# Performance work log

Measured on AMD Instinct MI355X. Metric: run time of the kernel, lower is better.

Reference implementation:

```python
import jax, jax.numpy as jnp
import numpy as np

# Static graph-batch geometry: B graphs, N nodes each (contiguous), DEG avg degree.
B, N, DEG = 128, 512, 16
GID, GH = 128, 128      # g_in_dim, g_hidden_dim
CID, CE = 64, 64        # c_in_dim, c_embed_dim
HAZ = 256               # haz_dim
K1, K2, K3 = 256, 128, 64


def _gcn(x, src, dst, mask, W, b, n):
    # GCN layer with self loops over masked (surviving) nodes; masked-out nodes contribute nothing.
    h = x @ W  # [n, GH]
    w = mask[src] * mask[dst]                                  # edge alive iff both endpoints alive
    deg = mask + jax.ops.segment_sum(w, dst, num_segments=n)    # +mask = self loop
    dinv = jax.lax.rsqrt(jnp.maximum(deg, 1.0))
    norm = w * dinv[src] * dinv[dst]
    agg = jax.ops.segment_sum(norm[:, None] * h[src], dst, num_segments=n)
    self_term = h * (mask * dinv * dinv)[:, None]               # self-loop norm = 1/deg
    return (agg + self_term + b) * mask[:, None]


def _pool(x, mask, p, k):
    # Score-based top-k pooling (MVPool score -> gate -> keep top ratio per graph), mask-based for static shapes.
    score = jax.nn.sigmoid((x @ p) / jnp.sqrt(jnp.sum(p * p)))  # [B*N]
    s = jnp.where(mask > 0, score, -jnp.inf).reshape(B, N)
    _, idx = jax.lax.top_k(s, k)                                 # [B, k]
    new_mask = jnp.zeros((B, N), x.dtype).at[jnp.arange(B)[:, None], idx].set(1.0).reshape(-1)
    x = x * (score * new_mask)[:, None]
    return x, new_mask


def _readout(x, mask):
    # readout='both': concat(global_max_pool, global_mean_pool) per graph.
    xm = x.reshape(B, N, -1)
    m = mask.reshape(B, N, 1)
    mx = jnp.max(jnp.where(m > 0, xm, -1e30), axis=1)
    avg = jnp.sum(xm * m, axis=1) / jnp.maximum(jnp.sum(m, axis=1), 1.0)
    return jnp.concatenate([mx, avg], axis=1)


def _forward(x, inp_c, src, dst, W1, b1, W2, b2, W3, b3, p1, p2, p3, We, Wa, ba, Wb, bb, Wc):
    n = B * N
    mask = jnp.ones((n,), x.dtype)
    x = jax.nn.relu(_gcn(x, src, dst, mask, W1, b1, n))
    x, mask = _pool(x, mask, p1, K1)
    x1 = _readout(x, mask)
    x = jax.nn.relu(_gcn(x, src, dst, mask, W2, b2, n))
    x, mask = _pool(x, mask, p2, K2)
    x2 = _readout(x, mask)
    x = jax.nn.relu(_gcn(x, src, dst, mask, W3, b3, n))
    x, mask = _pool(x, mask, p3, K3)
    x3 = _readout(x, mask)
    hg = jax.nn.relu(x1) + jax.nn.relu(x2) + jax.nn.relu(x3)     # [B, 2*GH]
    embed = jax.nn.relu(inp_c @ We)                               # [B, CE]
    fusion = jnp.concatenate([embed, hg], axis=1)                 # [B, 320]
    h = jax.nn.relu(fusion @ Wa + ba)                             # dropout skipped (eval mode)
    h = jax.nn.relu(h @ Wb + bb)
    return h @ Wc                                                 # out_dim=1 -> Identity


def setup_inputs() -> dict:
    key = jax.random.key(0)
    ks = jax.random.split(key, 16)
    n = B * N
    x = jax.random.normal(ks[0], (n, GID), jnp.float32)
    inp_c = jax.random.normal(ks[1], (B, CID), jnp.float32)
    offs = (jnp.arange(B, dtype=jnp.int32) * N)[:, None]
    src = (jax.random.randint(ks[2], (B, N * DEG), 0, N, jnp.int32) + offs).reshape(-1)
    dst = (jax.random.randint(ks[3], (B, N * DEG), 0, N, jnp.int32) + offs).reshape(-1)
    edge_index = jnp.stack([src, dst])
    batch = jnp.arange(n, dtype=jnp.int32) // N
    def lin(k, i, o):
        return jax.random.normal(k, (i, o), jnp.float32) / np.float32(np.sqrt(i))
    return dict(
        x=x, inp_c=inp_c, edge_index=edge_index, batch=batch,
        W1=lin(ks[4], GID, GH), b1=jnp.zeros((GH,), jnp.float32),
        W2=lin(ks[5], GH, GH), b2=jnp.zeros((GH,), jnp.float32),
        W3=lin(ks[6], GH, GH), b3=jnp.zeros((GH,), jnp.float32),
        p1=jax.random.normal(ks[7], (GH,), jnp.float32),
        p2=jax.random.normal(ks[8], (GH,), jnp.float32),
        p3=jax.random.normal(ks[9], (GH,), jnp.float32),
        We=lin(ks[10], CID, CE),
        Wa=lin(ks[11], 2 * GH + CE, HAZ), ba=jnp.zeros((HAZ,), jnp.float32),
        Wb=lin(ks[12], HAZ, HAZ // 2), bb=jnp.zeros((HAZ // 2,), jnp.float32),
        Wc=lin(ks[13], HAZ // 2, 1),
    )


def reference(x, inp_c, edge_index, batch, W1, b1, W2, b2, W3, b3, p1, p2, p3, We, Wa, ba, Wb, bb, Wc):
    # batch is implicitly arange(n)//N (contiguous equal-size graphs); reductions use the reshape form.
    src, dst = edge_index[0], edge_index[1]
    return _forward(x, inp_c, src, dst, W1, b1, W2, b2, W3, b3, p1, p2, p3, We, Wa, ba, Wb, bb, Wc)
```

## Files before the change

kernel.cpp:

```cpp
#include <hip/hip_runtime.h>
#include <math.h>

#define NNODE 65536
#define NEDGE 1048576
#define NGRAPH 128
#define NPG 512
#define EPG 8192

typedef _Float16 f16x8 __attribute__((ext_vector_type(8)));
typedef _Float16 f16x4 __attribute__((ext_vector_type(4)));
typedef float f32x4 __attribute__((ext_vector_type(4)));


__global__ __launch_bounds__(512) void k_csr(const int* __restrict__ srcE, const int* __restrict__ dstE,
                                             int* __restrict__ rp, int* __restrict__ csr,
                                             float* __restrict__ gate, int* __restrict__ alive,
                                             float* __restrict__ dinv) {
    __shared__ int cnt[512];
    __shared__ int tmp[512];
    int g = blockIdx.x, t = threadIdx.x;
    int nd = g * NPG + t;
    cnt[t] = 0;
    gate[nd] = 1.f;
    alive[nd] = nd;
    __syncthreads();
    int ebase = g * EPG;
    int dl[16];
    for (int i = 0; i < 16; ++i) {
        int e = ebase + t + i * 512;
        int d = dstE[e] - g * NPG;
        dl[i] = d;
        atomicAdd(&cnt[d], 1);
    }
    __syncthreads();
    int v = cnt[t], incl = v;
    dinv[nd] = rsqrtf(1.f + (float)v);
    for (int off = 1; off < 512; off <<= 1) {
        tmp[t] = incl; __syncthreads();
        if (t >= off) incl += tmp[t - off];
        __syncthreads();
    }
    int excl = incl - v;
    rp[nd] = ebase + excl;
    if (g == NGRAPH - 1 && t == 511) rp[NNODE] = NEDGE;
    __syncthreads();
    cnt[t] = excl;
    __syncthreads();
    for (int i = 0; i < 16; ++i) {
        int e = ebase + t + i * 512;
        int pos = atomicAdd(&cnt[dl[i]], 1);
        csr[ebase + pos] = srcE[e];
    }
}


__global__ __launch_bounds__(256) void k_wconv(const float* __restrict__ W0, const float* __restrict__ W1,
                                               const float* __restrict__ W2, _Float16* __restrict__ wh,
                                               _Float16* __restrict__ wl) {
    int l = blockIdx.x >> 6;
    int e = (blockIdx.x & 63) * 256 + threadIdx.x;
    const float* W = (l == 0) ? W0 : (l == 1) ? W1 : W2;
    int k = e >> 7, n = e & 127;
    float w = W[e];
    _Float16 hi = (_Float16)w;
    _Float16 lo = (_Float16)((w - (float)hi) * 2048.0f);
    int nt = n >> 4, nn = n & 15, ks = k >> 5, quad = (k & 31) >> 3, j = k & 7;
    int off = l * 16384 + ((nt * 4 + ks) * 64 + (quad * 16 + nn)) * 8 + j;
    wh[off] = hi;
    wl[off] = lo;
}


#define CVT8(hi8, lo8, a0, a1, a2, a3, a4, a5, a6, a7)                         \
    {                                                                           \
        _Float16 q0 = (_Float16)a0, q1 = (_Float16)a1, q2 = (_Float16)a2,       \
                 q3 = (_Float16)a3, q4 = (_Float16)a4, q5 = (_Float16)a5,       \
                 q6 = (_Float16)a6, q7 = (_Float16)a7;                          \
        hi8 = (f16x8){q0, q1, q2, q3, q4, q5, q6, q7};                          \
        lo8 = (f16x8){(_Float16)((a0 - (float)q0) * 2048.f),                    \
                      (_Float16)((a1 - (float)q1) * 2048.f),                    \
                      (_Float16)((a2 - (float)q2) * 2048.f),                    \
                      (_Float16)((a3 - (float)q3) * 2048.f),                    \
                      (_Float16)((a4 - (float)q4) * 2048.f),                    \
                      (_Float16)((a5 - (float)q5) * 2048.f),                    \
                      (_Float16)((a6 - (float)q6) * 2048.f),                    \
                      (_Float16)((a7 - (float)q7) * 2048.f)};                   \
    }

__global__ __launch_bounds__(256, 2) void k_gemm(const float* __restrict__ x0, const _Float16* __restrict__ xh,
                                                 const _Float16* __restrict__ xl, const _Float16* __restrict__ wh,
                                                 const _Float16* __restrict__ wl, const float* __restrict__ gate,
                                                 const int* __restrict__ alive, float* __restrict__ h,
                                                 int srcF32) {
    __shared__ _Float16 aH[128 * 72];
    __shared__ _Float16 aL[128 * 72];
    __shared__ _Float16 bH[8192];
    __shared__ _Float16 bL[8192];
    int t = threadIdx.x;
    int lane = t & 63;
    int wv = t >> 6;
    int quad = lane >> 4, mm = lane & 15;
    int rowbase = blockIdx.x * 128;

    f32x4 accH[2][8], accM[2][8];
    for (int a = 0; a < 2; ++a)
        for (int b = 0; b < 8; ++b) {
            accH[a][b] = (f32x4){0.f, 0.f, 0.f, 0.f};
            accM[a][b] = (f32x4){0.f, 0.f, 0.f, 0.f};
        }

    for (int kh = 0; kh < 2; ++kh) {
        if (kh) __syncthreads();
        for (int pp = 0; pp < 4; ++pp) {
            int seg = t + pp * 256;
            int nt = seg >> 7, ksl = (seg >> 6) & 1, ln = seg & 63;
            int goff = ((nt * 4 + kh * 2 + ksl) * 64 + ln) * 8;
            *(uint4*)(bH + seg * 8) = *(const uint4*)(wh + goff);
            *(uint4*)(bL + seg * 8) = *(const uint4*)(wl + goff);
        }
        for (int pp = 0; pp < 4; ++pp) {
            int c = t + pp * 256;
            int r = c >> 3, ch = c & 7;
            int node = alive[rowbase + r];
            size_t src = (size_t)node * 128 + kh * 64 + ch * 8;
            f16x8 hi8, lo8;
            if (srcF32) {
                float4 v0 = *(const float4*)(x0 + src);
                float4 v1 = *(const float4*)(x0 + src + 4);
                CVT8(hi8, lo8, v0.x, v0.y, v0.z, v0.w, v1.x, v1.y, v1.z, v1.w);
            } else {
                hi8 = *(const f16x8*)(xh + src);
                lo8 = *(const f16x8*)(xl + src);
            }
            *(f16x8*)(aH + r * 72 + ch * 8) = hi8;
            *(f16x8*)(aL + r * 72 + ch * 8) = lo8;
        }
        __syncthreads();

        for (int ksl = 0; ksl < 2; ++ksl) {
            f16x8 Ah[2], Al[2];
            for (int mt = 0; mt < 2; ++mt) {
                int row = wv * 32 + mt * 16 + mm;
                Ah[mt] = *(const f16x8*)(aH + row * 72 + ksl * 32 + quad * 8);
                Al[mt] = *(const f16x8*)(aL + row * 72 + ksl * 32 + quad * 8);
            }
            for (int nt = 0; nt < 8; ++nt) {
                f16x8 Bh = *(const f16x8*)(bH + ((nt * 2 + ksl) * 64 + lane) * 8);
                f16x8 Bl = *(const f16x8*)(bL + ((nt * 2 + ksl) * 64 + lane) * 8);
                for (int mt = 0; mt < 2; ++mt) {
                    accH[mt][nt] = __builtin_amdgcn_mfma_f32_16x16x32_f16(Ah[mt], Bh, accH[mt][nt], 0, 0, 0);
                    accM[mt][nt] = __builtin_amdgcn_mfma_f32_16x16x32_f16(Ah[mt], Bl, accM[mt][nt], 0, 0, 0);
                    accM[mt][nt] = __builtin_amdgcn_mfma_f32_16x16x32_f16(Al[mt], Bh, accM[mt][nt], 0, 0, 0);
                }
            }
        }
    }

    for (int mt = 0; mt < 2; ++mt)
        for (int i = 0; i < 4; ++i) {
            int rl = wv * 32 + mt * 16 + quad * 4 + i;
            int node = alive[rowbase + rl];
            float g = gate[node];
            float* hr = h + (size_t)node * 128 + mm;
            for (int nt = 0; nt < 8; ++nt)
                hr[nt * 16] = g * (accH[mt][nt][i] + accM[mt][nt][i] * (1.f / 2048.f));
        }
}


__global__ __launch_bounds__(256) void k_agg(const float* __restrict__ h, const float* __restrict__ dinv,
                                             const int* __restrict__ rp, const int* __restrict__ csr,
                                             const int* __restrict__ alive, const float* __restrict__ bias,
                                             const float* __restrict__ p, _Float16* __restrict__ xh,
                                             _Float16* __restrict__ xl, float* __restrict__ score, int Kp) {
    __shared__ float2 nb[8][16];
    int t = threadIdx.x;
    int slot = t >> 5;
    int lane32 = t & 31;
    int half = slot & 1;
    int g = blockIdx.x & 127;
    int chunk = blockIdx.x >> 7;
    int idx = chunk * 8 + slot;

    int d = alive[g * Kp + idx];
    int jb = rp[d];
    int je = rp[d + 1];
    int deg = je - jb;

    int sid = 0; float wv = 0.f; bool livej = false;
    if (lane32 < 16 && lane32 < deg) {
        sid = csr[jb + lane32];
        wv = dinv[sid];
        livej = (wv != 0.f);
    }
    unsigned long long bal = __ballot(livej);
    unsigned hm = (unsigned)((bal >> (half * 32)) & 0xFFFFu);
    int cnt = __popc(hm);
    if (livej) {
        int pos = __popc(hm & ((1u << lane32) - 1));
        nb[slot][pos] = make_float2(wv, __int_as_float(sid));
    }

    float dvd = dinv[d];
    float4 hd = *(const float4*)(h + (size_t)d * 128 + lane32 * 4);
    float4 a0, a1;
    a0.x = dvd * hd.x; a0.y = dvd * hd.y; a0.z = dvd * hd.z; a0.w = dvd * hd.w;
    a1.x = 0.f; a1.y = 0.f; a1.z = 0.f; a1.w = 0.f;

    int j = 0;
    for (; j + 2 <= cnt; j += 2) {
        float2 n0 = nb[slot][j];
        float2 n1 = nb[slot][j + 1];
        int s0 = __float_as_int(n0.y);
        int s1 = __float_as_int(n1.y);
        float4 h0 = *(const float4*)(h + (size_t)s0 * 128 + lane32 * 4);
        float4 h1 = *(const float4*)(h + (size_t)s1 * 128 + lane32 * 4);
        a0.x = fmaf(n0.x, h0.x, a0.x); a0.y = fmaf(n0.x, h0.y, a0.y);
        a0.z = fmaf(n0.x, h0.z, a0.z); a0.w = fmaf(n0.x, h0.w, a0.w);
        a1.x = fmaf(n1.x, h1.x, a1.x); a1.y = fmaf(n1.x, h1.y, a1.y);
        a1.z = fmaf(n1.x, h1.z, a1.z); a1.w = fmaf(n1.x, h1.w, a1.w);
    }
    if (j < cnt) {
        float2 n0 = nb[slot][j];
        int s0 = __float_as_int(n0.y);
        float4 h0 = *(const float4*)(h + (size_t)s0 * 128 + lane32 * 4);
        a0.x = fmaf(n0.x, h0.x, a0.x); a0.y = fmaf(n0.x, h0.y, a0.y);
        a0.z = fmaf(n0.x, h0.z, a0.z); a0.w = fmaf(n0.x, h0.w, a0.w);
    }
    for (int j2 = jb + 16; j2 < je; ++j2) {
        int s2 = csr[j2];
        float w2 = dinv[s2];
        float4 h2 = *(const float4*)(h + (size_t)s2 * 128 + lane32 * 4);
        a0.x = fmaf(w2, h2.x, a0.x); a0.y = fmaf(w2, h2.y, a0.y);
        a0.z = fmaf(w2, h2.z, a0.z); a0.w = fmaf(w2, h2.w, a0.w);
    }

    float4 b4 = *(const float4*)(bias + lane32 * 4);
    float4 o;
    o.x = fmaxf(fmaf(dvd, a0.x + a1.x, b4.x), 0.f);
    o.y = fmaxf(fmaf(dvd, a0.y + a1.y, b4.y), 0.f);
    o.z = fmaxf(fmaf(dvd, a0.z + a1.z, b4.z), 0.f);
    o.w = fmaxf(fmaf(dvd, a0.w + a1.w, b4.w), 0.f);

    _Float16 q0 = (_Float16)o.x, q1 = (_Float16)o.y, q2 = (_Float16)o.z, q3 = (_Float16)o.w;
    f16x4 oh = {q0, q1, q2, q3};
    f16x4 ol = {(_Float16)((o.x - (float)q0) * 2048.f), (_Float16)((o.y - (float)q1) * 2048.f),
                (_Float16)((o.z - (float)q2) * 2048.f), (_Float16)((o.w - (float)q3) * 2048.f)};
    *(f16x4*)(xh + (size_t)d * 128 + lane32 * 4) = oh;
    *(f16x4*)(xl + (size_t)d * 128 + lane32 * 4) = ol;

    float4 p4 = *(const float4*)(p + lane32 * 4);
    float ps = o.x * p4.x + o.y * p4.y + o.z * p4.z + o.w * p4.w;
    float q = p4.x * p4.x + p4.y * p4.y + p4.z * p4.z + p4.w * p4.w;
    for (int m = 16; m >= 1; m >>= 1) {
        ps += __shfl_xor(ps, m);
        q += __shfl_xor(q, m);
    }
    if (lane32 == 0) score[d] = 1.f / (1.f + expf(-ps * rsqrtf(q)));
}


__global__ __launch_bounds__(512) void k_pool(const _Float16* __restrict__ xh, const _Float16* __restrict__ xl,
                                              const float* __restrict__ score, float* __restrict__ gate,
                                              int* __restrict__ alive, float* __restrict__ hg,
                                              const int* __restrict__ rp, const int* __restrict__ csr,
                                              float* __restrict__ dinv, int K, int last) {
    __shared__ float s[512];
    __shared__ int ad[256];
    __shared__ float ag[256];
    __shared__ float red[1024];
    __shared__ int m_new[512];
    __shared__ int scnt;
    int t = threadIdx.x, g = blockIdx.x;
    int gbase = g * NPG;
    int d = gbase + t;

    float odv = dinv[d];
    int m = odv > 0.f;
    float sc = score[d];
    if (t == 0) scnt = 0;
    s[t] = m ? sc : -__builtin_inff();
    __syncthreads();
    for (int k2 = 2; k2 <= 512; k2 <<= 1)
        for (int j = k2 >> 1; j > 0; j >>= 1) {
            int ixj = t ^ j;
            if (ixj > t) {
                float a = s[t], bv = s[ixj];
                bool sw = ((t & k2) == 0) ? (a < bv) : (a > bv);
                if (sw) { s[t] = bv; s[ixj] = a; }
            }
            __syncthreads();
        }
    float thr = s[K - 1];
    int nm = (m && sc >= thr) ? 1 : 0;
    gate[d] = nm ? sc : 0.f;
    m_new[t] = nm;
    if (nm) {
        int pos = atomicAdd(&scnt, 1);
        if (pos < K) {
            alive[g * K + pos] = d;
            ad[pos] = d;
            ag[pos] = sc;
        }
    }
    __syncthreads();

    if (!last) {
        float nd = 0.f;
        if (nm) {
            int jb = rp[d], je = rp[d + 1];
            int sum = 0;
            for (int j = jb; j < je; ++j) sum += m_new[csr[j] - gbase];
            nd = rsqrtf(1.f + (float)sum);
        }
        dinv[d] = nd;
    }

    int f = t & 127, c = t >> 7;
    float mx = 0.f, sm = 0.f;
#define REC(node) ((float)xh[(size_t)(node)*128 + f] + (float)xl[(size_t)(node)*128 + f] * (1.f / 2048.f))
    for (int j = c; j < K; j += 16) {
        float v0 = REC(ad[j]) * ag[j];
        float v1 = REC(ad[j + 4]) * ag[j + 4];
        float v2 = REC(ad[j + 8]) * ag[j + 8];
        float v3 = REC(ad[j + 12]) * ag[j + 12];
        mx = fmaxf(fmaxf(fmaxf(mx, v0), fmaxf(v1, v2)), v3);
        sm += v0 + v1 + v2 + v3;
    }
#undef REC
    red[t] = mx; red[512 + t] = sm;
    __syncthreads();
    if (c == 0) {
        for (int cc = 1; cc < 4; ++cc) {
            mx = fmaxf(mx, red[cc * 128 + f]);
            sm += red[512 + cc * 128 + f];
        }
        hg[g * 256 + f] += mx;
        hg[g * 256 + 128 + f] += sm / (float)K;
    }
}


__global__ __launch_bounds__(256) void k_mlp(const float* __restrict__ inp_c, const float* __restrict__ hg,
                                             const float* __restrict__ We, const float* __restrict__ Wa,
                                             const float* __restrict__ ba, const float* __restrict__ Wb,
                                             const float* __restrict__ bb, const float* __restrict__ Wc,
                                             float* __restrict__ out) {
    __shared__ float fus[320];
    __shared__ float h1[256];
    __shared__ float h2[128];
    int t = threadIdx.x, g = blockIdx.x;
    if (t < 64) {
        float a = 0.f;
        for (int j = 0; j < 64; ++j) a = fmaf(inp_c[g * 64 + j], We[j * 64 + t], a);
        fus[t] = fmaxf(a, 0.f);
    }
    fus[64 + t] = hg[g * 256 + t];
    __syncthreads();
    {
        float a = ba[t];
        for (int j = 0; j < 320; ++j) a = fmaf(fus[j], Wa[j * 256 + t], a);
        h1[t] = fmaxf(a, 0.f);
    }
    __syncthreads();
    if (t < 128) {
        float a = bb[t];
        for (int j = 0; j < 256; ++j) a = fmaf(h1[j], Wb[j * 128 + t], a);
        h2[t] = fmaxf(a, 0.f);
    }
    __syncthreads();
    if (t == 0) {
        float a = 0.f;
        for (int j = 0; j < 128; ++j) a = fmaf(h2[j], Wc[j], a);
        out[g] = a;
    }
}


extern "C" void kernel_launch(void* const* d_in, const int* in_sizes, int n_in,
                              void* d_out, int out_size, void* d_ws, size_t ws_size,
                              hipStream_t stream) {
    (void)in_sizes; (void)n_in; (void)out_size; (void)ws_size;
    const float* x_in  = (const float*)d_in[0];
    const float* inp_c = (const float*)d_in[1];
    const int*   ei    = (const int*)d_in[2];
    const int* srcE = ei;
    const int* dstE = ei + NEDGE;
    const float* Wl[3] = {(const float*)d_in[4], (const float*)d_in[6], (const float*)d_in[8]};
    const float* bl[3] = {(const float*)d_in[5], (const float*)d_in[7], (const float*)d_in[9]};
    const float* Pl[3] = {(const float*)d_in[10], (const float*)d_in[11], (const float*)d_in[12]};
    const float* We = (const float*)d_in[13];
    const float* Wa = (const float*)d_in[14];
    const float* ba = (const float*)d_in[15];
    const float* Wb = (const float*)d_in[16];
    const float* bb = (const float*)d_in[17];
    const float* Wc = (const float*)d_in[18];
    float* out = (float*)d_out;

    char* w = (char*)d_ws;
    size_t off = 0;
    auto alloc = [&](size_t bytes) -> void* {
        void* p = w + off;
        off = (off + bytes + 255) & ~(size_t)255;
        return p;
    };
    int*   rp    = (int*)alloc((NNODE + 1) * 4);
    int*   csr   = (int*)alloc(NEDGE * 4);
    float* dinv  = (float*)alloc(NNODE * 4);
    float* gate  = (float*)alloc(NNODE * 4);
    float* score = (float*)alloc(NNODE * 4);
    int*   alive = (int*)alloc(NNODE * 4);
    float* hbuf  = (float*)alloc((size_t)NNODE * 128 * 4);
    _Float16* xh = (_Float16*)alloc((size_t)NNODE * 128 * 2);
    _Float16* xl = (_Float16*)alloc((size_t)NNODE * 128 * 2);
    float* hg    = (float*)alloc(NGRAPH * 256 * 4);
    _Float16* wfh = (_Float16*)alloc(3 * 16384 * 2);
    _Float16* wfl = (_Float16*)alloc(3 * 16384 * 2);

    hipMemsetAsync(hg, 0, NGRAPH * 256 * 4, stream);
    k_wconv<<<192, 256, 0, stream>>>(Wl[0], Wl[1], Wl[2], wfh, wfl);
    k_csr<<<NGRAPH, 512, 0, stream>>>(srcE, dstE, rp, csr, gate, alive, dinv);

    const int rows_in[3] = {65536, 32768, 16384};
    const int Ks[3] = {256, 128, 64};
    const int Kp[3] = {512, 256, 128};
    for (int l = 0; l < 3; ++l) {
        k_gemm<<<rows_in[l] / 128, 256, 0, stream>>>(x_in, xh, xl, wfh + l * 16384, wfl + l * 16384,
                                                     gate, alive, hbuf, l == 0);
        k_agg<<<rows_in[l] / 8, 256, 0, stream>>>(hbuf, dinv, rp, csr, alive, bl[l], Pl[l],
                                                  xh, xl, score, Kp[l]);
        k_pool<<<NGRAPH, 512, 0, stream>>>(xh, xl, score, gate, alive, hg,
                                           rp, csr, dinv, Ks[l], l == 2);
    }
    k_mlp<<<NGRAPH, 256, 0, stream>>>(inp_c, hg, We, Wa, ba, Wb, bb, Wc, out);
}
```

Baseline: 309.8 us.

## Replace bitonic sort top-k with radix histogram select; widen aggregation neighbor staging

The pooling kernel no longer runs a full 512-element bitonic sort, which needs about 45 block barriers, to find the K-th largest score. It now builds a 1024-bucket histogram on the top bits of each score, prefix-scans it to locate the bucket holding the K-th value, and ranks only the candidates in that bucket. The aggregation kernel stages up to 32 neighbors per node in shared memory instead of 16, and unrolls the gather loop by 4 with four accumulators to keep more loads in flight. The risks are shared-memory atomic contention when many scores fall in one bucket, and a quadratic candidate ranking if scores cluster. Tied scores at the threshold could also be handled differently from the sort.

```diff
diff --git a/kernel.cpp b/kernel.cpp
--- a/kernel.cpp
+++ b/kernel.cpp
@@ -173,7 +173,7 @@
                                              const int* __restrict__ alive, const float* __restrict__ bias,
                                              const float* __restrict__ p, _Float16* __restrict__ xh,
                                              _Float16* __restrict__ xl, float* __restrict__ score, int Kp) {
-    __shared__ float2 nb[8][16];
+    __shared__ float2 nb[8][32];
     int t = threadIdx.x;
     int slot = t >> 5;
     int lane32 = t & 31;
@@ -188,13 +188,13 @@
     int deg = je - jb;
 
     int sid = 0; float wv = 0.f; bool livej = false;
-    if (lane32 < 16 && lane32 < deg) {
+    if (lane32 < deg) {
         sid = csr[jb + lane32];
         wv = dinv[sid];
         livej = (wv != 0.f);
     }
     unsigned long long bal = __ballot(livej);
-    unsigned hm = (unsigned)((bal >> (half * 32)) & 0xFFFFu);
+    unsigned hm = (unsigned)(bal >> (half * 32));
     int cnt = __popc(hm);
     if (livej) {
         int pos = __popc(hm & ((1u << lane32) - 1));
@@ -203,31 +203,37 @@
 
     float dvd = dinv[d];
     float4 hd = *(const float4*)(h + (size_t)d * 128 + lane32 * 4);
-    float4 a0, a1;
+    float4 a0, a1, a2, a3;
     a0.x = dvd * hd.x; a0.y = dvd * hd.y; a0.z = dvd * hd.z; a0.w = dvd * hd.w;
-    a1.x = 0.f; a1.y = 0.f; a1.z = 0.f; a1.w = 0.f;
+    a1 = make_float4(0.f, 0.f, 0.f, 0.f);
+    a2 = a1; a3 = a1;
 
     int j = 0;
-    for (; j + 2 <= cnt; j += 2) {
+    for (; j + 4 <= cnt; j += 4) {
         float2 n0 = nb[slot][j];
         float2 n1 = nb[slot][j + 1];
-        int s0 = __float_as_int(n0.y);
-        int s1 = __float_as_int(n1.y);
-        float4 h0 = *(const float4*)(h + (size_t)s0 * 128 + lane32 * 4);
-        float4 h1 = *(const float4*)(h + (size_t)s1 * 128 + lane32 * 4);
+        float2 n2 = nb[slot][j + 2];
+        float2 n3 = nb[slot][j + 3];
+        float4 h0 = *(const float4*)(h + (size_t)__float_as_int(n0.y) * 128 + lane32 * 4);
+        float4 h1 = *(const float4*)(h + (size_t)__float_as_int(n1.y) * 128 + lane32 * 4);
+        float4 h2 = *(const float4*)(h + (size_t)__float_as_int(n2.y) * 128 + lane32 * 4);
+        float4 h3 = *(const float4*)(h + (size_t)__float_as_int(n3.y) * 128 + lane32 * 4);
         a0.x = fmaf(n0.x, h0.x, a0.x); a0.y = fmaf(n0.x, h0.y, a0.y);
         a0.z = fmaf(n0.x, h0.z, a0.z); a0.w = fmaf(n0.x, h0.w, a0.w);
         a1.x = fmaf(n1.x, h1.x, a1.x); a1.y = fmaf(n1.x, h1.y, a1.y);
         a1.z = fmaf(n1.x, h1.z, a1.z); a1.w = fmaf(n1.x, h1.w, a1.w);
-    }
-    if (j < cnt) {
+        a2.x = fmaf(n2.x, h2.x, a2.x); a2.y = fmaf(n2.x, h2.y, a2.y);
+        a2.z = fmaf(n2.x, h2.z, a2.z); a2.w = fmaf(n2.x, h2.w, a2.w);
+        a3.x = fmaf(n3.x, h3.x, a3.x); a3.y = fmaf(n3.x, h3.y, a3.y);
+        a3.z = fmaf(n3.x, h3.z, a3.z); a3.w = fmaf(n3.x, h3.w, a3.w);
+    }
+    for (; j < cnt; ++j) {
         float2 n0 = nb[slot][j];
-        int s0 = __float_as_int(n0.y);
-        float4 h0 = *(const float4*)(h + (size_t)s0 * 128 + lane32 * 4);
+        float4 h0 = *(const float4*)(h + (size_t)__float_as_int(n0.y) * 128 + lane32 * 4);
         a0.x = fmaf(n0.x, h0.x, a0.x); a0.y = fmaf(n0.x, h0.y, a0.y);
         a0.z = fmaf(n0.x, h0.z, a0.z); a0.w = fmaf(n0.x, h0.w, a0.w);
     }
-    for (int j2 = jb + 16; j2 < je; ++j2) {
+    for (int j2 = jb + 32; j2 < je; ++j2) {
         int s2 = csr[j2];
         float w2 = dinv[s2];
         float4 h2 = *(const float4*)(h + (size_t)s2 * 128 + lane32 * 4);
@@ -237,10 +243,10 @@
 
     float4 b4 = *(const float4*)(bias + lane32 * 4);
     float4 o;
-    o.x = fmaxf(fmaf(dvd, a0.x + a1.x, b4.x), 0.f);
-    o.y = fmaxf(fmaf(dvd, a0.y + a1.y, b4.y), 0.f);
-    o.z = fmaxf(fmaf(dvd, a0.z + a1.z, b4.z), 0.f);
-    o.w = fmaxf(fmaf(dvd, a0.w + a1.w, b4.w), 0.f);
+    o.x = fmaxf(fmaf(dvd, a0.x + a1.x + a2.x + a3.x, b4.x), 0.f);
+    o.y = fmaxf(fmaf(dvd, a0.y + a1.y + a2.y + a3.y, b4.y), 0.f);
+    o.z = fmaxf(fmaf(dvd, a0.z + a1.z + a2.z + a3.z, b4.z), 0.f);
+    o.w = fmaxf(fmaf(dvd, a0.w + a1.w + a2.w + a3.w, b4.w), 0.f);
 
     _Float16 q0 = (_Float16)o.x, q1 = (_Float16)o.y, q2 = (_Float16)o.z, q3 = (_Float16)o.w;
     f16x4 oh = {q0, q1, q2, q3};
@@ -265,12 +271,17 @@
                                               int* __restrict__ alive, float* __restrict__ hg,
                                               const int* __restrict__ rp, const int* __restrict__ csr,
                                               float* __restrict__ dinv, int K, int last) {
-    __shared__ float s[512];
+    __shared__ unsigned hist[1024];
+    __shared__ unsigned wsum[8];
+    __shared__ float cand[512];
     __shared__ int ad[256];
     __shared__ float ag[256];
     __shared__ float red[1024];
     __shared__ int m_new[512];
     __shared__ int scnt;
+    __shared__ unsigned ccnt;
+    __shared__ unsigned tbb, tbab;
+    __shared__ float thrS;
     int t = threadIdx.x, g = blockIdx.x;
     int gbase = g * NPG;
     int d = gbase + t;
@@ -278,20 +289,51 @@
     float odv = dinv[d];
     int m = odv > 0.f;
     float sc = score[d];
-    if (t == 0) scnt = 0;
-    s[t] = m ? sc : -__builtin_inff();
-    __syncthreads();
-    for (int k2 = 2; k2 <= 512; k2 <<= 1)
-        for (int j = k2 >> 1; j > 0; j >>= 1) {
-            int ixj = t ^ j;
-            if (ixj > t) {
-                float a = s[t], bv = s[ixj];
-                bool sw = ((t & k2) == 0) ? (a < bv) : (a > bv);
-                if (sw) { s[t] = bv; s[ixj] = a; }
-            }
-            __syncthreads();
-        }
-    float thr = s[K - 1];
+    unsigned bits = m ? __float_as_uint(sc) : 0u;
+    unsigned bucket = bits >> 21;
+    hist[t] = 0; hist[t + 512] = 0;
+    if (t == 0) { scnt = 0; ccnt = 0; }
+    __syncthreads();
+    atomicAdd(&hist[bucket], 1u);
+    __syncthreads();
+    unsigned a0 = hist[1023 - 2 * t];
+    unsigned a1 = hist[1022 - 2 * t];
+    unsigned pair = a0 + a1;
+    unsigned v = pair;
+    for (int o = 1; o < 64; o <<= 1) {
+        unsigned n = __shfl_up(v, o);
+        if ((t & 63) >= o) v += n;
+    }
+    if ((t & 63) == 63) wsum[t >> 6] = v;
+    __syncthreads();
+    if (t == 0) {
+        unsigned run = 0;
+        for (int i = 0; i < 8; ++i) { unsigned x = wsum[i]; wsum[i] = run; run += x; }
+    }
+    __syncthreads();
+    unsigned incl = v + wsum[t >> 6];
+    unsigned excl = incl - pair;
+    unsigned uK = (unsigned)K;
+    if (excl < uK && excl + a0 >= uK) { tbb = 1023 - 2 * t; tbab = excl; }
+    else if (excl + a0 < uK && incl >= uK) { tbb = 1022 - 2 * t; tbab = excl + a0; }
+    __syncthreads();
+    unsigned bsel = tbb;
+    unsigned r = uK - tbab;
+    if (m && bucket == bsel) {
+        unsigned pos = atomicAdd(&ccnt, 1u);
+        cand[pos] = sc;
+    }
+    __syncthreads();
+    unsigned c = ccnt;
+    if (t < (int)c) {
+        float vv = cand[t];
+        unsigned gt = 0;
+        for (unsigned i = 0; i < c; ++i) gt += (cand[i] > vv) ? 1u : 0u;
+        if (gt == r - 1) thrS = vv;
+    }
+    __syncthreads();
+    float thr = thrS;
+
     int nm = (m && sc >= thr) ? 1 : 0;
     gate[d] = nm ? sc : 0.f;
     m_new[t] = nm;
@@ -316,10 +358,10 @@
         dinv[d] = nd;
     }
 
-    int f = t & 127, c = t >> 7;
+    int f = t & 127, c2 = t >> 7;
     float mx = 0.f, sm = 0.f;
 #define REC(node) ((float)xh[(size_t)(node)*128 + f] + (float)xl[(size_t)(node)*128 + f] * (1.f / 2048.f))
-    for (int j = c; j < K; j += 16) {
+    for (int j = c2; j < K; j += 16) {
         float v0 = REC(ad[j]) * ag[j];
         float v1 = REC(ad[j + 4]) * ag[j + 4];
         float v2 = REC(ad[j + 8]) * ag[j + 8];
@@ -330,7 +372,7 @@
 #undef REC
     red[t] = mx; red[512 + t] = sm;
     __syncthreads();
-    if (c == 0) {
+    if (c2 == 0) {
         for (int cc = 1; cc < 4; ++cc) {
             mx = fmaxf(mx, red[cc * 128 + f]);
             sm += red[512 + cc * 128 + f];
```

Result: faster. 289.8 us (-6.5%).
